# Performance work log

Measured on AMD Instinct MI355X. Metric: run time of the kernel, lower is better.

Reference implementation:

```python
import jax, jax.numpy as jnp
import numpy as np


def _conv(x, w, pad):
    return jax.lax.conv_general_dilated(x, w, (1, 1), [(pad, pad), (pad, pad)],
                                        dimension_numbers=('NCHW', 'OIHW', 'NCHW'))


def _cbs(x, w, s, b, pad):
    # Conv + (folded inference BatchNorm as per-channel affine) + SiLU
    y = _conv(x, w, pad) * s[None, :, None, None] + b[None, :, None, None]
    return y * jax.nn.sigmoid(y)


def _pixel_shuffle(x, r):
    N, C, H, W = x.shape
    c = C // (r * r)
    return x.reshape(N, c, r, r, H, W).transpose(0, 1, 4, 2, 5, 3).reshape(N, c, H * r, W * r)


def _pixel_unshuffle(x, r):
    N, C, H, W = x.shape
    h, w = H // r, W // r
    return x.reshape(N, C, h, r, w, r).transpose(0, 1, 3, 5, 2, 4).reshape(N, C * r * r, h, w)


def _carafe(x, dw, db, ew, eb, k, up):
    # Content-aware reassembly: predict per-pixel k*k kernels for up*up sub-positions,
    # softmax-normalize, then gather-multiply-accumulate over k*k neighborhoods.
    N, C, H, W = x.shape
    kt = _conv(x, dw, 0) + db[None, :, None, None]
    if k % 2 == 0:
        kt = jnp.pad(kt, ((0, 0), (0, 0), (k // 2, k // 2 - 1), (k // 2, k // 2 - 1)))
        kt = _conv(kt, ew, 0) + eb[None, :, None, None]
    else:
        kt = _conv(kt, ew, k // 2) + eb[None, :, None, None]
    kt = _pixel_shuffle(kt, up)                     # [N, k*k, H*up, W*up]
    kt = jax.nn.softmax(kt, axis=1)
    # non-overlapping unfold(step=up) -> [N, H, W, k*k, up*up]
    kt = kt.reshape(N, k * k, H, up, W, up).transpose(0, 2, 4, 1, 3, 5).reshape(N, H, W, k * k, up * up)
    if k % 2 == 0:
        xp = jnp.pad(x, ((0, 0), (0, 0), (k // 2, k // 2 - 1), (k // 2, k // 2 - 1)))
    else:
        xp = jnp.pad(x, ((0, 0), (0, 0), (k // 2, k // 2), (k // 2, k // 2)))
    # k*k sliding patches (k is a small static constant)
    patches = jnp.stack([xp[:, :, i:i + H, j:j + W] for i in range(k) for j in range(k)], axis=-1)
    patches = patches.transpose(0, 2, 3, 1, 4)      # [N, H, W, C, k*k]
    out = jnp.einsum('nhwck,nhwkr->nhwcr', patches, kt)  # [N, H, W, C, up*up]
    out = out.reshape(N, H, W, C * up * up).transpose(0, 3, 1, 2)
    return _pixel_shuffle(out, up)


def _forward(x, cv1_w, cv1_s, cv1_b, m1a_w, m1a_s, m1a_b, m1b_w, m1b_s, m1b_b,
             cvm2_w, cvm2_s, cvm2_b, u2_down_w, u2_down_b, u2_enc_w, u2_enc_b,
             m2a_w, m2a_s, m2a_b, m2b_w, m2b_s, m2b_b,
             cvm3_w, cvm3_s, cvm3_b, u3_down_w, u3_down_b, u3_enc_w, u3_enc_b,
             m3a_w, m3a_s, m3a_b, m3b_w, m3b_s, m3b_b, cv2_w, cv2_s, cv2_b):
    C = cv1_w.shape[0] // 2
    t = _cbs(x, cv1_w, cv1_s, cv1_b, 0)
    y, y0 = t[:, :C], t[:, C:]

    def bneck(z, wa, sa, ba, wb, sb, bb):  # shortcut=False, e=1.0
        return _cbs(_cbs(z, wa, sa, ba, 1), wb, sb, bb, 1)

    y1 = bneck(y0, m1a_w, m1a_s, m1a_b, m1b_w, m1b_s, m1b_b)
    y2 = _cbs(_pixel_unshuffle(y1, 2), cvm2_w, cvm2_s, cvm2_b, 0)
    y2 = _carafe(y2, u2_down_w, u2_down_b, u2_enc_w, u2_enc_b, 1, 2) + y1
    y2 = bneck(y2, m2a_w, m2a_s, m2a_b, m2b_w, m2b_s, m2b_b)
    y3 = _cbs(_pixel_unshuffle(y2, 4), cvm3_w, cvm3_s, cvm3_b, 0)
    y3 = _carafe(y3, u3_down_w, u3_down_b, u3_enc_w, u3_enc_b, 2, 4) + y2
    y3 = bneck(y3, m3a_w, m3a_s, m3a_b, m3b_w, m3b_s, m3b_b)
    return _cbs(jnp.concatenate([y, y0, y1, y2, y3], axis=1), cv2_w, cv2_s, cv2_b, 0)


def setup_inputs() -> dict:
    key = jax.random.key(0)
    ks = jax.random.split(key, 16)
    C = 128

    def cbs_p(k, co, ci, ksz):
        k1, k2, k3 = jax.random.split(k, 3)
        w = jax.random.normal(k1, (co, ci, ksz, ksz), jnp.float32) / np.sqrt(ci * ksz * ksz).astype(np.float32)
        s = 1.0 + 0.1 * jax.random.normal(k2, (co,), jnp.float32)
        b = 0.1 * jax.random.normal(k3, (co,), jnp.float32)
        return w, s, b

    d = {}
    d['x'] = jax.random.normal(ks[0], (8, 256, 128, 128), jnp.float32)
    d['cv1_w'], d['cv1_s'], d['cv1_b'] = cbs_p(ks[1], 2 * C, 256, 1)
    for name, kk in (('m1', ks[2]), ('m2', ks[3]), ('m3', ks[4])):
        ka, kb = jax.random.split(kk)
        d[name + 'a_w'], d[name + 'a_s'], d[name + 'a_b'] = cbs_p(ka, C, C, 3)
        d[name + 'b_w'], d[name + 'b_s'], d[name + 'b_b'] = cbs_p(kb, C, C, 3)
    d['cvm2_w'], d['cvm2_s'], d['cvm2_b'] = cbs_p(ks[5], C, 4 * C, 1)
    d['cvm3_w'], d['cvm3_s'], d['cvm3_b'] = cbs_p(ks[6], C, 16 * C, 1)
    d['u2_down_w'] = jax.random.normal(ks[7], (C // 4, C, 1, 1), jnp.float32) / np.sqrt(C).astype(np.float32)
    d['u2_down_b'] = 0.1 * jax.random.normal(ks[8], (C // 4,), jnp.float32)
    d['u2_enc_w'] = jax.random.normal(ks[9], (4, C // 4, 1, 1), jnp.float32) / np.sqrt(C // 4).astype(np.float32)
    d['u2_enc_b'] = 0.1 * jax.random.normal(ks[10], (4,), jnp.float32)
    d['u3_down_w'] = jax.random.normal(ks[11], (C // 4, C, 1, 1), jnp.float32) / np.sqrt(C).astype(np.float32)
    d['u3_down_b'] = 0.1 * jax.random.normal(ks[12], (C // 4,), jnp.float32)
    d['u3_enc_w'] = jax.random.normal(ks[13], (64, C // 4, 2, 2), jnp.float32) / np.sqrt((C // 4) * 4).astype(np.float32)
    d['u3_enc_b'] = 0.1 * jax.random.normal(ks[14], (64,), jnp.float32)
    d['cv2_w'], d['cv2_s'], d['cv2_b'] = cbs_p(ks[15], 256, 5 * C, 1)
    return d


def reference(x, cv1_w, cv1_s, cv1_b, m1a_w, m1a_s, m1a_b, m1b_w, m1b_s, m1b_b,
              cvm2_w, cvm2_s, cvm2_b, u2_down_w, u2_down_b, u2_enc_w, u2_enc_b,
              m2a_w, m2a_s, m2a_b, m2b_w, m2b_s, m2b_b,
              cvm3_w, cvm3_s, cvm3_b, u3_down_w, u3_down_b, u3_enc_w, u3_enc_b,
              m3a_w, m3a_s, m3a_b, m3b_w, m3b_s, m3b_b, cv2_w, cv2_s, cv2_b):
    return _forward(x, cv1_w, cv1_s, cv1_b, m1a_w, m1a_s, m1a_b, m1b_w, m1b_s, m1b_b,
                    cvm2_w, cvm2_s, cvm2_b, u2_down_w, u2_down_b, u2_enc_w, u2_enc_b,
                    m2a_w, m2a_s, m2a_b, m2b_w, m2b_s, m2b_b,
                    cvm3_w, cvm3_s, cvm3_b, u3_down_w, u3_down_b, u3_enc_w, u3_enc_b,
                    m3a_w, m3a_s, m3a_b, m3b_w, m3b_s, m3b_b, cv2_w, cv2_s, cv2_b)
```

## Files before the change

### kernel.cpp

```cpp
#include <hip/hip_runtime.h>

typedef unsigned short u16;
typedef short v8s __attribute__((ext_vector_type(8)));
typedef u16 v8u __attribute__((ext_vector_type(8)));
typedef float v4f __attribute__((ext_vector_type(4)));
typedef __bf16 v8bf __attribute__((ext_vector_type(8)));

__device__ __forceinline__ float bf2f(u16 u) {
    unsigned x = ((unsigned)u) << 16; float f; __builtin_memcpy(&f, &x, 4); return f;
}
__device__ __forceinline__ u16 f2bf(float f) {
    unsigned x; __builtin_memcpy(&x, &f, 4);
    x = x + 0x7FFFu + ((x >> 16) & 1u);
    return (u16)(x >> 16);
}
__device__ __forceinline__ float silu(float v) { return v / (1.f + __expf(-v)); }

__global__ void cvtw(const float* __restrict__ in, u16* __restrict__ out, int n) {
    int i = blockIdx.x * 256 + threadIdx.x;
    if (i < n) out[i] = f2bf(in[i]);
}
__global__ void wtrans3(const float* __restrict__ in, u16* __restrict__ out) {
    int i = blockIdx.x * 256 + threadIdx.x;
    if (i >= 147456) return;
    int tap = i % 9; int rem = i / 9; int ci = rem & 127; int co = rem >> 7;
    out[((tap * 128 + co) << 7) + ci] = f2bf(in[i]);
}
__global__ void wtrans_ps(const float* __restrict__ in, u16* __restrict__ out, int R2) {
    int i = blockIdx.x * 256 + threadIdx.x;
    int tap = i % R2; int rem = i / R2; int c = rem & 127; int co = rem >> 7;
    out[((tap * 128 + co) << 7) + c] = f2bf(in[i]);
}

__global__ __launch_bounds__(256) void nchw2nhwc(const float* __restrict__ in, u16* __restrict__ out) {
    __shared__ u16 tile[64][72];
    const int n = blockIdx.z, c0 = blockIdx.y * 64, p0 = blockIdx.x * 64;
#pragma unroll
    for (int rep = 0; rep < 16; ++rep) {
        int idx = rep * 256 + threadIdx.x;
        int c = idx >> 6, p = idx & 63;
        tile[c][p] = f2bf(in[((size_t)(n * 256 + c0 + c)) * 16384 + p0 + p]);
    }
    __syncthreads();
#pragma unroll
    for (int rep = 0; rep < 16; ++rep) {
        int idx = rep * 256 + threadIdx.x;
        int p = idx >> 6, c = idx & 63;
        out[((size_t)n * 16384 + p0 + p) * 256 + c0 + c] = tile[c][p];
    }
}

__global__ __launch_bounds__(256) void conv3_mfma(
    const u16* __restrict__ src, int c0, int srcC,
    const u16* __restrict__ wt,
    const float* __restrict__ scale, const float* __restrict__ bias,
    u16* __restrict__ out) {
    __shared__ u16 lds[3][128][40];
    const int n = blockIdx.y, h = blockIdx.x;
    const int tid = threadIdx.x;
    const int lane = tid & 63;
    const int wv = tid >> 6;
    const int r = lane & 15, q = lane >> 4;
    const int wr = wv >> 1, wc = wv & 1;

    v4f acc[4][4];
#pragma unroll
    for (int a = 0; a < 4; ++a)
#pragma unroll
        for (int b = 0; b < 4; ++b) acc[a][b] = (v4f){0.f, 0.f, 0.f, 0.f};

    const size_t rowstride = (size_t)128 * srcC;
    const u16* nbase = src + (size_t)n * 128 * rowstride + c0;

    for (int k0 = 0; k0 < 128; k0 += 32) {
        __syncthreads();
#pragma unroll
        for (int kh = 0; kh < 3; ++kh) {
            int hh = h + kh - 1;
            if ((unsigned)hh < 128u) {
                const u16* g = nbase + (size_t)hh * rowstride + k0;
#pragma unroll
                for (int it = 0; it < 2; ++it) {
                    int t = it * 256 + tid;
                    v8s val = *(const v8s*)(g + (size_t)(t >> 2) * srcC + (t & 3) * 8);
                    *(v8s*)&lds[kh][t >> 2][(t & 3) * 8] = val;
                }
            }
        }
        __syncthreads();
#pragma unroll
        for (int kh = 0; kh < 3; ++kh) {
            int hh = h + kh - 1;
            if ((unsigned)hh >= 128u) continue;
#pragma unroll
            for (int kw = 0; kw < 3; ++kw) {
                int tap = kh * 3 + kw;
                const u16* bb = wt + ((size_t)tap * 128 + wc * 64 + r) * 128 + k0 + q * 8;
                v8bf bfr[4];
#pragma unroll
                for (int nt = 0; nt < 4; ++nt)
                    bfr[nt] = __builtin_bit_cast(v8bf, *(const v8s*)(bb + nt * 16 * 128));
                v8bf afr[4];
#pragma unroll
                for (int mt = 0; mt < 4; ++mt) {
                    int p = wr * 64 + mt * 16 + r + kw - 1;
                    bool vp = (unsigned)p < 128u;
                    int pc = vp ? p : 0;
                    v8s av = *(const v8s*)&lds[kh][pc][q * 8];
                    if (!vp) av = (v8s){0, 0, 0, 0, 0, 0, 0, 0};
                    afr[mt] = __builtin_bit_cast(v8bf, av);
                }
#pragma unroll
                for (int mt = 0; mt < 4; ++mt)
#pragma unroll
                    for (int nt = 0; nt < 4; ++nt)
                        acc[mt][nt] = __builtin_amdgcn_mfma_f32_16x16x32_bf16(
                            afr[mt], bfr[nt], acc[mt][nt], 0, 0, 0);
            }
        }
    }

    const size_t obase = ((size_t)n * 128 + h) * 128;
#pragma unroll
    for (int nt = 0; nt < 4; ++nt) {
        int co = wc * 64 + nt * 16 + r;
        float s = scale[co], bi = bias[co];
#pragma unroll
        for (int mt = 0; mt < 4; ++mt) {
            int p = wr * 64 + mt * 16 + q * 4;
#pragma unroll
            for (int i = 0; i < 4; ++i) {
                float v = acc[mt][nt][i] * s + bi;
                out[(obase + p + i) * 128 + co] = f2bf(silu(v));
            }
        }
    }
}

__global__ __launch_bounds__(256) void conv1_mfma(
    const u16* __restrict__ src, int srcC,
    const u16* __restrict__ wt,
    const float* __restrict__ scale, const float* __restrict__ bias,
    u16* __restrict__ out, int Cout) {
    __shared__ u16 lds[128][40];
    const int n = blockIdx.z, co0 = blockIdx.y * 128, px0 = blockIdx.x * 128;
    const int tid = threadIdx.x;
    const int lane = tid & 63, wv = tid >> 6;
    const int r = lane & 15, q = lane >> 4;
    const int wr = wv >> 1, wc = wv & 1;

    v4f acc[4][4];
#pragma unroll
    for (int a = 0; a < 4; ++a)
#pragma unroll
        for (int b = 0; b < 4; ++b) acc[a][b] = (v4f){0.f, 0.f, 0.f, 0.f};

    const u16* abase = src + ((size_t)n * 16384 + px0) * srcC;

    for (int k0 = 0; k0 < srcC; k0 += 32) {
        __syncthreads();
#pragma unroll
        for (int it = 0; it < 2; ++it) {
            int t = it * 256 + tid;
            v8s val = *(const v8s*)(abase + (size_t)(t >> 2) * srcC + (t & 3) * 8 + k0);
            *(v8s*)&lds[t >> 2][(t & 3) * 8] = val;
        }
        __syncthreads();
        const u16* bb = wt + (size_t)(co0 + wc * 64 + r) * srcC + k0 + q * 8;
        v8bf bfr[4];
#pragma unroll
        for (int nt = 0; nt < 4; ++nt)
            bfr[nt] = __builtin_bit_cast(v8bf, *(const v8s*)(bb + (size_t)nt * 16 * srcC));
        v8bf afr[4];
#pragma unroll
        for (int mt = 0; mt < 4; ++mt)
            afr[mt] = __builtin_bit_cast(v8bf, *(const v8s*)&lds[wr * 64 + mt * 16 + r][q * 8]);
#pragma unroll
        for (int mt = 0; mt < 4; ++mt)
#pragma unroll
            for (int nt = 0; nt < 4; ++nt)
                acc[mt][nt] = __builtin_amdgcn_mfma_f32_16x16x32_bf16(
                    afr[mt], bfr[nt], acc[mt][nt], 0, 0, 0);
    }

#pragma unroll
    for (int nt = 0; nt < 4; ++nt) {
        int co = co0 + wc * 64 + nt * 16 + r;
        float s = scale[co], bi = bias[co];
#pragma unroll
        for (int mt = 0; mt < 4; ++mt) {
            int p = px0 + wr * 64 + mt * 16 + q * 4;
#pragma unroll
            for (int i = 0; i < 4; ++i) {
                float v = acc[mt][nt][i] * s + bi;
                out[((size_t)n * 16384 + p + i) * Cout + co] = f2bf(silu(v));
            }
        }
    }
}

__global__ __launch_bounds__(256) void cat_mfma(
    const u16* __restrict__ s0, const u16* __restrict__ s1,
    const u16* __restrict__ s2, const u16* __restrict__ s3,
    const u16* __restrict__ wt,
    const float* __restrict__ scale, const float* __restrict__ bias,
    float* __restrict__ out) {
    __shared__ u16 lds[128][40];
    const int n = blockIdx.z, co0 = blockIdx.y * 128, px0 = blockIdx.x * 128;
    const int tid = threadIdx.x;
    const int lane = tid & 63, wv = tid >> 6;
    const int r = lane & 15, q = lane >> 4;
    const int wr = wv >> 1, wc = wv & 1;

    v4f acc[4][4];
#pragma unroll
    for (int a = 0; a < 4; ++a)
#pragma unroll
        for (int b = 0; b < 4; ++b) acc[a][b] = (v4f){0.f, 0.f, 0.f, 0.f};

    const u16* srcs[4] = {s0, s1, s2, s3};
    const int sCq[4] = {256, 128, 128, 128};
    const int kbq[4] = {0, 256, 384, 512};

#pragma unroll
    for (int seg = 0; seg < 4; ++seg) {
        const int sc = sCq[seg];
        const u16* ab = srcs[seg] + ((size_t)n * 16384 + px0) * sc;
        for (int k0 = 0; k0 < sc; k0 += 32) {
            __syncthreads();
#pragma unroll
            for (int it = 0; it < 2; ++it) {
                int t = it * 256 + tid;
                v8s val = *(const v8s*)(ab + (size_t)(t >> 2) * sc + (t & 3) * 8 + k0);
                *(v8s*)&lds[t >> 2][(t & 3) * 8] = val;
            }
            __syncthreads();
            const u16* bb = wt + (size_t)(co0 + wc * 64 + r) * 640 + kbq[seg] + k0 + q * 8;
            v8bf bfr[4];
#pragma unroll
            for (int nt = 0; nt < 4; ++nt)
                bfr[nt] = __builtin_bit_cast(v8bf, *(const v8s*)(bb + nt * 16 * 640));
            v8bf afr[4];
#pragma unroll
            for (int mt = 0; mt < 4; ++mt)
                afr[mt] = __builtin_bit_cast(v8bf, *(const v8s*)&lds[wr * 64 + mt * 16 + r][q * 8]);
#pragma unroll
            for (int mt = 0; mt < 4; ++mt)
#pragma unroll
                for (int nt = 0; nt < 4; ++nt)
                    acc[mt][nt] = __builtin_amdgcn_mfma_f32_16x16x32_bf16(
                        afr[mt], bfr[nt], acc[mt][nt], 0, 0, 0);
        }
    }

#pragma unroll
    for (int nt = 0; nt < 4; ++nt) {
        int co = co0 + wc * 64 + nt * 16 + r;
        float s = scale[co], bi = bias[co];
#pragma unroll
        for (int mt = 0; mt < 4; ++mt) {
            int p = px0 + wr * 64 + mt * 16 + q * 4;
            v4f o;
#pragma unroll
            for (int i = 0; i < 4; ++i) o[i] = silu(acc[mt][nt][i] * s + bi);
            *(v4f*)(out + (size_t)(n * 256 + co) * 16384 + p) = o;
        }
    }
}

template <int KH, int KW, int S, int PAD, int CIN>
__global__ __launch_bounds__(256) void conv_mfma(
    const u16* __restrict__ src, int c0, int srcC,
    const u16* __restrict__ wt,
    const float* __restrict__ scale, const float* __restrict__ bias,
    u16* __restrict__ out, int Hin, int Win, int Wout, int Cout) {
    const int n = blockIdx.z;
    const int co0 = blockIdx.y * 64;
    const int hw0 = blockIdx.x * 64;
    const int tid = threadIdx.x;
    const int lane = tid & 63, wv = tid >> 6;
    const int r = lane & 15, q = lane >> 4;
    const int wr = wv >> 1, wc = wv & 1;

    const int m0 = hw0 + wr * 32 + r;
    const int m1 = m0 + 16;
    const int h0 = m0 / Wout, w0 = m0 - h0 * Wout;
    const int h1 = m1 / Wout, w1 = m1 - h1 * Wout;

    v4f acc00 = {0.f, 0.f, 0.f, 0.f}, acc01 = {0.f, 0.f, 0.f, 0.f};
    v4f acc10 = {0.f, 0.f, 0.f, 0.f}, acc11 = {0.f, 0.f, 0.f, 0.f};

    const u16* b0base = wt + (size_t)(co0 + wc * 32 + r) * CIN + q * 8;
    const size_t wtap = (size_t)Cout * CIN;

    int tap = 0;
#pragma unroll
    for (int kh = 0; kh < KH; ++kh)
#pragma unroll
        for (int kw = 0; kw < KW; ++kw, ++tap) {
            int ih0 = h0 * S + kh - PAD, iw0 = w0 * S + kw - PAD;
            int ih1 = h1 * S + kh - PAD, iw1 = w1 * S + kw - PAD;
            bool v0 = ((unsigned)ih0 < (unsigned)Hin) & ((unsigned)iw0 < (unsigned)Win);
            bool v1 = ((unsigned)ih1 < (unsigned)Hin) & ((unsigned)iw1 < (unsigned)Win);
            int p0i = v0 ? (n * Hin + ih0) * Win + iw0 : 0;
            int p1i = v1 ? (n * Hin + ih1) * Win + iw1 : 0;
            const u16* a0 = src + (size_t)p0i * srcC + c0 + q * 8;
            const u16* a1 = src + (size_t)p1i * srcC + c0 + q * 8;
            const u16* b0 = b0base + (size_t)tap * wtap;
            const u16* b1 = b0 + (size_t)16 * CIN;
#pragma unroll
            for (int k = 0; k < CIN; k += 32) {
                v8s za = {0, 0, 0, 0, 0, 0, 0, 0};
                v8s a0s = za, a1s = za;
                if (v0) a0s = *(const v8s*)(a0 + k);
                if (v1) a1s = *(const v8s*)(a1 + k);
                v8s b0s = *(const v8s*)(b0 + k);
                v8s b1s = *(const v8s*)(b1 + k);
                v8bf af0 = __builtin_bit_cast(v8bf, a0s);
                v8bf af1 = __builtin_bit_cast(v8bf, a1s);
                v8bf bw0 = __builtin_bit_cast(v8bf, b0s);
                v8bf bw1 = __builtin_bit_cast(v8bf, b1s);
                acc00 = __builtin_amdgcn_mfma_f32_16x16x32_bf16(af0, bw0, acc00, 0, 0, 0);
                acc01 = __builtin_amdgcn_mfma_f32_16x16x32_bf16(af0, bw1, acc01, 0, 0, 0);
                acc10 = __builtin_amdgcn_mfma_f32_16x16x32_bf16(af1, bw0, acc10, 0, 0, 0);
                acc11 = __builtin_amdgcn_mfma_f32_16x16x32_bf16(af1, bw1, acc11, 0, 0, 0);
            }
        }

    const int HWo = gridDim.x * 64;
#pragma unroll
    for (int ct = 0; ct < 2; ++ct) {
        v4f av0 = ct ? acc01 : acc00;
        v4f av1 = ct ? acc11 : acc10;
        int co = co0 + wc * 32 + ct * 16 + r;
        float s = scale[co], bb = bias[co];
        int mb = hw0 + wr * 32 + q * 4;
#pragma unroll
        for (int i = 0; i < 4; ++i) {
            float x0 = av0[i] * s + bb;
            float x1 = av1[i] * s + bb;
            out[((size_t)n * HWo + mb + i) * Cout + co] = f2bf(silu(x0));
            out[((size_t)n * HWo + mb + 16 + i) * Cout + co] = f2bf(silu(x1));
        }
    }
}

__global__ __launch_bounds__(256) void k_upadd(const u16* __restrict__ y2a,
                                               const u16* __restrict__ y1,
                                               u16* __restrict__ out) {
    int t = blockIdx.x * 256 + threadIdx.x;
    int cg = t & 15; int pix = t >> 4;
    int n = pix >> 14; int p = pix & 16383; int ho = p >> 7; int wo = p & 127;
    const u16* a = y2a + ((size_t)((n * 64 + (ho >> 1)) * 64 + (wo >> 1))) * 128 + cg * 8;
    const u16* b = y1 + (size_t)pix * 128 + cg * 8;
    v8s av = *(const v8s*)a;
    v8s bv = *(const v8s*)b;
    v8u o;
#pragma unroll
    for (int e = 0; e < 8; ++e) o[e] = f2bf(bf2f((u16)av[e]) + bf2f((u16)bv[e]));
    *(v8u*)(out + (size_t)pix * 128 + cg * 8) = o;
}

__global__ __launch_bounds__(256) void k_u3down(const u16* __restrict__ y3a,
                                                const float* __restrict__ w,
                                                const float* __restrict__ b,
                                                float* __restrict__ ktA) {
    int t = blockIdx.x * 256 + threadIdx.x;
    int co = t & 31; int pix = t >> 5;
    const u16* xr = y3a + (size_t)pix * 128;
    const float* wr = w + (size_t)co * 128;
    float acc = b[co];
#pragma unroll 16
    for (int k = 0; k < 128; ++k) acc += bf2f(xr[k]) * wr[k];
    ktA[t] = acc;
}

__global__ __launch_bounds__(256) void k_u3enc(const float* __restrict__ ktA,
                                               const float* __restrict__ ew,
                                               const float* __restrict__ eb,
                                               float* __restrict__ wtsm) {
    int t = blockIdx.x * 256 + threadIdx.x;
    int r = t & 15; int pix = t >> 4;
    int n = pix >> 10; int hw = pix & 1023; int h = hw >> 5; int w = hw & 31;
    float v[4];
#pragma unroll
    for (int kk = 0; kk < 4; ++kk) {
        int co = kk * 16 + r;
        float acc = eb[co];
#pragma unroll
        for (int dh = 0; dh < 2; ++dh)
#pragma unroll
            for (int dw = 0; dw < 2; ++dw) {
                int hh = h - 1 + dh, ww = w - 1 + dw;
                if (hh < 0 || ww < 0) continue;
                const float* kp = ktA + ((size_t)((n * 32 + hh) * 32 + ww)) * 32;
                const float* wp = ew + (size_t)co * 128 + dh * 2 + dw;
                for (int ci = 0; ci < 32; ++ci) acc += kp[ci] * wp[ci * 4];
            }
        v[kk] = acc;
    }
    float mx = fmaxf(fmaxf(v[0], v[1]), fmaxf(v[2], v[3]));
    float e0 = __expf(v[0] - mx), e1 = __expf(v[1] - mx), e2 = __expf(v[2] - mx), e3 = __expf(v[3] - mx);
    float inv = 1.f / (e0 + e1 + e2 + e3);
    float* o = wtsm + (size_t)t * 4;
    o[0] = e0 * inv; o[1] = e1 * inv; o[2] = e2 * inv; o[3] = e3 * inv;
}

__global__ __launch_bounds__(256) void k_carafe(const u16* __restrict__ y3a,
                                                const float* __restrict__ wtsm,
                                                const u16* __restrict__ y2,
                                                u16* __restrict__ out) {
    int t = blockIdx.x * 256 + threadIdx.x;
    int cg = t & 15; int pix = t >> 4;
    int n = pix >> 14; int p = pix & 16383; int ho = p >> 7; int wo = p & 127;
    int h = ho >> 2, i = ho & 3, w = wo >> 2, j = wo & 3, r = i * 4 + j;
    const float* wv = wtsm + ((size_t)((n * 1024 + h * 32 + w) * 16 + r)) * 4;
    v8s yv = *(const v8s*)(y2 + (size_t)pix * 128 + cg * 8);
    float acc[8];
#pragma unroll
    for (int e = 0; e < 8; ++e) acc[e] = bf2f((u16)yv[e]);
#pragma unroll
    for (int kk = 0; kk < 4; ++kk) {
        int ki = kk >> 1, kj = kk & 1;
        int hh = h + ki - 1, ww = w + kj - 1;
        if (hh < 0 || ww < 0) continue;
        float wk = wv[kk];
        v8s sv = *(const v8s*)(y3a + ((size_t)((n * 32 + hh) * 32 + ww)) * 128 + cg * 8);
#pragma unroll
        for (int e = 0; e < 8; ++e) acc[e] += wk * bf2f((u16)sv[e]);
    }
    v8u o;
#pragma unroll
    for (int e = 0; e < 8; ++e) o[e] = f2bf(acc[e]);
    *(v8u*)(out + (size_t)pix * 128 + cg * 8) = o;
}

extern "C" void kernel_launch(void* const* d_in, const int* in_sizes, int n_in,
                              void* d_out, int out_size, void* d_ws, size_t ws_size,
                              hipStream_t stream) {
    const float* x     = (const float*)d_in[0];
    const float* cv1_w = (const float*)d_in[1];
    const float* cv1_s = (const float*)d_in[2];
    const float* cv1_b = (const float*)d_in[3];
    const float* m1a_w = (const float*)d_in[4];
    const float* m1a_s = (const float*)d_in[5];
    const float* m1a_b = (const float*)d_in[6];
    const float* m1b_w = (const float*)d_in[7];
    const float* m1b_s = (const float*)d_in[8];
    const float* m1b_b = (const float*)d_in[9];
    const float* m2a_w = (const float*)d_in[10];
    const float* m2a_s = (const float*)d_in[11];
    const float* m2a_b = (const float*)d_in[12];
    const float* m2b_w = (const float*)d_in[13];
    const float* m2b_s = (const float*)d_in[14];
    const float* m2b_b = (const float*)d_in[15];
    const float* m3a_w = (const float*)d_in[16];
    const float* m3a_s = (const float*)d_in[17];
    const float* m3a_b = (const float*)d_in[18];
    const float* m3b_w = (const float*)d_in[19];
    const float* m3b_s = (const float*)d_in[20];
    const float* m3b_b = (const float*)d_in[21];
    const float* cvm2_w = (const float*)d_in[22];
    const float* cvm2_s = (const float*)d_in[23];
    const float* cvm2_b = (const float*)d_in[24];
    const float* cvm3_w = (const float*)d_in[25];
    const float* cvm3_s = (const float*)d_in[26];
    const float* cvm3_b = (const float*)d_in[27];
    const float* u3_down_w = (const float*)d_in[32];
    const float* u3_down_b = (const float*)d_in[33];
    const float* u3_enc_w  = (const float*)d_in[34];
    const float* u3_enc_b  = (const float*)d_in[35];
    const float* cv2_w = (const float*)d_in[36];
    const float* cv2_s = (const float*)d_in[37];
    const float* cv2_b = (const float*)d_in[38];

    char* ws = (char*)d_ws;
    u16* A    = (u16*)(ws + 0);
    u16* t    = (u16*)(ws + 67108864);
    u16* y1   = (u16*)(ws + 134217728);
    u16* bt   = (u16*)(ws + 167772160);
    u16* te   = (u16*)(ws + 201326592);
    u16* y2a  = (u16*)(ws + 234881024);
    u16* y3a  = (u16*)(ws + 243269632);
    float* ktA = (float*)(ws + 245366784);
    float* wts = (float*)(ws + 246415360);
    u16* w3t  = (u16*)(ws + 248512512);
    u16* wu2  = (u16*)(ws + 250281984);
    u16* wu4  = (u16*)(ws + 250413056);
    u16* wc1  = (u16*)(ws + 250937344);
    u16* wc2  = (u16*)(ws + 251068416);
    u16* y2 = A;
    u16* y3 = A + 16777216;

    dim3 B(256);
    wtrans3<<<576, B, 0, stream>>>(m1a_w, w3t + 0 * 147456);
    wtrans3<<<576, B, 0, stream>>>(m1b_w, w3t + 1 * 147456);
    wtrans3<<<576, B, 0, stream>>>(m2a_w, w3t + 2 * 147456);
    wtrans3<<<576, B, 0, stream>>>(m2b_w, w3t + 3 * 147456);
    wtrans3<<<576, B, 0, stream>>>(m3a_w, w3t + 4 * 147456);
    wtrans3<<<576, B, 0, stream>>>(m3b_w, w3t + 5 * 147456);
    wtrans_ps<<<256, B, 0, stream>>>(cvm2_w, wu2, 4);
    wtrans_ps<<<1024, B, 0, stream>>>(cvm3_w, wu4, 16);
    cvtw<<<256, B, 0, stream>>>(cv1_w, wc1, 65536);
    cvtw<<<640, B, 0, stream>>>(cv2_w, wc2, 163840);

    nchw2nhwc<<<dim3(256, 4, 8), B, 0, stream>>>(x, A);

    conv1_mfma<<<dim3(128, 2, 8), B, 0, stream>>>(A, 256, wc1, cv1_s, cv1_b, t, 256);

    conv3_mfma<<<dim3(128, 8), B, 0, stream>>>(t, 128, 256, w3t + 0 * 147456, m1a_s, m1a_b, bt);
    conv3_mfma<<<dim3(128, 8), B, 0, stream>>>(bt, 0, 128, w3t + 1 * 147456, m1b_s, m1b_b, y1);

    conv_mfma<2, 2, 2, 0, 128><<<dim3(64, 2, 8), B, 0, stream>>>(
        y1, 0, 128, wu2, cvm2_s, cvm2_b, y2a, 128, 128, 64, 128);

    k_upadd<<<8192, B, 0, stream>>>(y2a, y1, te);

    conv3_mfma<<<dim3(128, 8), B, 0, stream>>>(te, 0, 128, w3t + 2 * 147456, m2a_s, m2a_b, bt);
    conv3_mfma<<<dim3(128, 8), B, 0, stream>>>(bt, 0, 128, w3t + 3 * 147456, m2b_s, m2b_b, y2);

    conv_mfma<4, 4, 4, 0, 128><<<dim3(16, 2, 8), B, 0, stream>>>(
        y2, 0, 128, wu4, cvm3_s, cvm3_b, y3a, 128, 128, 32, 128);

    k_u3down<<<1024, B, 0, stream>>>(y3a, u3_down_w, u3_down_b, ktA);
    k_u3enc<<<512, B, 0, stream>>>(ktA, u3_enc_w, u3_enc_b, wts);
    k_carafe<<<8192, B, 0, stream>>>(y3a, wts, y2, te);

    conv3_mfma<<<dim3(128, 8), B, 0, stream>>>(te, 0, 128, w3t + 4 * 147456, m3a_s, m3a_b, bt);
    conv3_mfma<<<dim3(128, 8), B, 0, stream>>>(bt, 0, 128, w3t + 5 * 147456, m3b_s, m3b_b, y3);

    cat_mfma<<<dim3(128, 2, 8), B, 0, stream>>>(t, y1, y2, y3, wc2, cv2_s, cv2_b, (float*)d_out);
}
```

Before: 1.400 ms.

## Use direct global-to-LDS loads and widen K tile in conv GEMM kernels

Replaces the register-staged global-to-shared copies in the 3x3 conv, 1x1 conv and concat GEMM kernels with global_load_lds 16-byte direct transfers into unpadded LDS tiles. The 1x1 and concat kernels also move from a K step of 32 to 64, which halves the number of barrier pairs per reduction. Dropping the LDS row padding to fit the contiguous layout that direct loads need can bring back bank conflicts on the fragment reads.

```diff
diff --git a/kernel.cpp b/kernel.cpp
--- a/kernel.cpp
+++ b/kernel.cpp
@@ -16,6 +16,13 @@
 }
 __device__ __forceinline__ float silu(float v) { return v / (1.f + __expf(-v)); }
 
+__device__ __forceinline__ void gld16(const void* g, void* l) {
+    __builtin_amdgcn_global_load_lds(
+        (const __attribute__((address_space(1))) unsigned int*)(uintptr_t)g,
+        (__attribute__((address_space(3))) unsigned int*)(unsigned int)(uintptr_t)l,
+        16, 0, 0);
+}
+
 __global__ void cvtw(const float* __restrict__ in, u16* __restrict__ out, int n) {
     int i = blockIdx.x * 256 + threadIdx.x;
     if (i < n) out[i] = f2bf(in[i]);
@@ -55,7 +62,7 @@
     const u16* __restrict__ wt,
     const float* __restrict__ scale, const float* __restrict__ bias,
     u16* __restrict__ out) {
-    __shared__ u16 lds[3][128][40];
+    __shared__ u16 lds[3][128][32];
     const int n = blockIdx.y, h = blockIdx.x;
     const int tid = threadIdx.x;
     const int lane = tid & 63;
@@ -80,10 +87,11 @@
             if ((unsigned)hh < 128u) {
                 const u16* g = nbase + (size_t)hh * rowstride + k0;
 #pragma unroll
-                for (int it = 0; it < 2; ++it) {
-                    int t = it * 256 + tid;
-                    v8s val = *(const v8s*)(g + (size_t)(t >> 2) * srcC + (t & 3) * 8);
-                    *(v8s*)&lds[kh][t >> 2][(t & 3) * 8] = val;
+                for (int j = 0; j < 2; ++j) {
+                    int o = j * 4096 + tid * 16;
+                    int px = o >> 6, cb = o & 63;
+                    gld16((const char*)(g + (size_t)px * srcC) + cb,
+                          (char*)&lds[kh][0][0] + j * 4096 + wv * 1024);
                 }
             }
         }
@@ -142,7 +150,7 @@
     const u16* __restrict__ wt,
     const float* __restrict__ scale, const float* __restrict__ bias,
     u16* __restrict__ out, int Cout) {
-    __shared__ u16 lds[128][40];
+    __shared__ u16 lds[128][64];
     const int n = blockIdx.z, co0 = blockIdx.y * 128, px0 = blockIdx.x * 128;
     const int tid = threadIdx.x;
     const int lane = tid & 63, wv = tid >> 6;
@@ -157,30 +165,34 @@
 
     const u16* abase = src + ((size_t)n * 16384 + px0) * srcC;
 
-    for (int k0 = 0; k0 < srcC; k0 += 32) {
+    for (int k0 = 0; k0 < srcC; k0 += 64) {
         __syncthreads();
 #pragma unroll
-        for (int it = 0; it < 2; ++it) {
-            int t = it * 256 + tid;
-            v8s val = *(const v8s*)(abase + (size_t)(t >> 2) * srcC + (t & 3) * 8 + k0);
-            *(v8s*)&lds[t >> 2][(t & 3) * 8] = val;
+        for (int j = 0; j < 4; ++j) {
+            int o = j * 4096 + tid * 16;
+            int px = o >> 7, cb = o & 127;
+            gld16((const char*)(abase + (size_t)px * srcC + k0) + cb,
+                  (char*)&lds[0][0] + j * 4096 + wv * 1024);
         }
         __syncthreads();
-        const u16* bb = wt + (size_t)(co0 + wc * 64 + r) * srcC + k0 + q * 8;
-        v8bf bfr[4];
-#pragma unroll
-        for (int nt = 0; nt < 4; ++nt)
-            bfr[nt] = __builtin_bit_cast(v8bf, *(const v8s*)(bb + (size_t)nt * 16 * srcC));
-        v8bf afr[4];
-#pragma unroll
-        for (int mt = 0; mt < 4; ++mt)
-            afr[mt] = __builtin_bit_cast(v8bf, *(const v8s*)&lds[wr * 64 + mt * 16 + r][q * 8]);
-#pragma unroll
-        for (int mt = 0; mt < 4; ++mt)
+#pragma unroll
+        for (int s = 0; s < 2; ++s) {
+            const u16* bb = wt + (size_t)(co0 + wc * 64 + r) * srcC + k0 + s * 32 + q * 8;
+            v8bf bfr[4];
 #pragma unroll
             for (int nt = 0; nt < 4; ++nt)
-                acc[mt][nt] = __builtin_amdgcn_mfma_f32_16x16x32_bf16(
-                    afr[mt], bfr[nt], acc[mt][nt], 0, 0, 0);
+                bfr[nt] = __builtin_bit_cast(v8bf, *(const v8s*)(bb + (size_t)nt * 16 * srcC));
+            v8bf afr[4];
+#pragma unroll
+            for (int mt = 0; mt < 4; ++mt)
+                afr[mt] = __builtin_bit_cast(v8bf, *(const v8s*)&lds[wr * 64 + mt * 16 + r][s * 32 + q * 8]);
+#pragma unroll
+            for (int mt = 0; mt < 4; ++mt)
+#pragma unroll
+                for (int nt = 0; nt < 4; ++nt)
+                    acc[mt][nt] = __builtin_amdgcn_mfma_f32_16x16x32_bf16(
+                        afr[mt], bfr[nt], acc[mt][nt], 0, 0, 0);
+        }
     }
 
 #pragma unroll
@@ -205,7 +217,7 @@
     const u16* __restrict__ wt,
     const float* __restrict__ scale, const float* __restrict__ bias,
     float* __restrict__ out) {
-    __shared__ u16 lds[128][40];
+    __shared__ u16 lds[128][64];
     const int n = blockIdx.z, co0 = blockIdx.y * 128, px0 = blockIdx.x * 128;
     const int tid = threadIdx.x;
     const int lane = tid & 63, wv = tid >> 6;
@@ -226,30 +238,34 @@
     for (int seg = 0; seg < 4; ++seg) {
         const int sc = sCq[seg];
         const u16* ab = srcs[seg] + ((size_t)n * 16384 + px0) * sc;
-        for (int k0 = 0; k0 < sc; k0 += 32) {
+        for (int k0 = 0; k0 < sc; k0 += 64) {
             __syncthreads();
 #pragma unroll
-            for (int it = 0; it < 2; ++it) {
-                int t = it * 256 + tid;
-                v8s val = *(const v8s*)(ab + (size_t)(t >> 2) * sc + (t & 3) * 8 + k0);
-                *(v8s*)&lds[t >> 2][(t & 3) * 8] = val;
+            for (int j = 0; j < 4; ++j) {
+                int o = j * 4096 + tid * 16;
+                int px = o >> 7, cb = o & 127;
+                gld16((const char*)(ab + (size_t)px * sc + k0) + cb,
+                      (char*)&lds[0][0] + j * 4096 + wv * 1024);
             }
             __syncthreads();
-            const u16* bb = wt + (size_t)(co0 + wc * 64 + r) * 640 + kbq[seg] + k0 + q * 8;
-            v8bf bfr[4];
-#pragma unroll
-            for (int nt = 0; nt < 4; ++nt)
-                bfr[nt] = __builtin_bit_cast(v8bf, *(const v8s*)(bb + nt * 16 * 640));
-            v8bf afr[4];
-#pragma unroll
-            for (int mt = 0; mt < 4; ++mt)
-                afr[mt] = __builtin_bit_cast(v8bf, *(const v8s*)&lds[wr * 64 + mt * 16 + r][q * 8]);
-#pragma unroll
-            for (int mt = 0; mt < 4; ++mt)
+#pragma unroll
+            for (int s = 0; s < 2; ++s) {
+                const u16* bb = wt + (size_t)(co0 + wc * 64 + r) * 640 + kbq[seg] + k0 + s * 32 + q * 8;
+                v8bf bfr[4];
 #pragma unroll
                 for (int nt = 0; nt < 4; ++nt)
-                    acc[mt][nt] = __builtin_amdgcn_mfma_f32_16x16x32_bf16(
-                        afr[mt], bfr[nt], acc[mt][nt], 0, 0, 0);
+                    bfr[nt] = __builtin_bit_cast(v8bf, *(const v8s*)(bb + nt * 16 * 640));
+                v8bf afr[4];
+#pragma unroll
+                for (int mt = 0; mt < 4; ++mt)
+                    afr[mt] = __builtin_bit_cast(v8bf, *(const v8s*)&lds[wr * 64 + mt * 16 + r][s * 32 + q * 8]);
+#pragma unroll
+                for (int mt = 0; mt < 4; ++mt)
+#pragma unroll
+                    for (int nt = 0; nt < 4; ++nt)
+                        acc[mt][nt] = __builtin_amdgcn_mfma_f32_16x16x32_bf16(
+                            afr[mt], bfr[nt], acc[mt][nt], 0, 0, 0);
+            }
         }
     }
 
```

Result: faster. 1.354 ms (-3.3%).

## Drop LDS staging in conv kernels and load MFMA operands directly from global

Applied to the files above, without the earlier changes.

Removes shared-memory staging and the __syncthreads barriers from the 3x3 conv, 1x1 conv and concat GEMM kernels, so each lane reads its A-fragments straight from global memory (relying on L1/L2 for reuse across waves). The 1x1 kernel also processes two 32-wide K slices per loop iteration. This removes barrier stalls and LDS traffic, but increases global/cache load traffic: each A row is read by both column-waves, and the 3x3 kernel re-reads rows per kw shift.

```diff
diff --git a/kernel.cpp b/kernel.cpp
--- a/kernel.cpp
+++ b/kernel.cpp
@@ -55,11 +55,9 @@
     const u16* __restrict__ wt,
     const float* __restrict__ scale, const float* __restrict__ bias,
     u16* __restrict__ out) {
-    __shared__ u16 lds[3][128][40];
     const int n = blockIdx.y, h = blockIdx.x;
     const int tid = threadIdx.x;
-    const int lane = tid & 63;
-    const int wv = tid >> 6;
+    const int lane = tid & 63, wv = tid >> 6;
     const int r = lane & 15, q = lane >> 4;
     const int wr = wv >> 1, wc = wv & 1;
 
@@ -72,30 +70,23 @@
     const size_t rowstride = (size_t)128 * srcC;
     const u16* nbase = src + (size_t)n * 128 * rowstride + c0;
 
+    bool rv[3];
+    const u16* row[3];
+#pragma unroll
+    for (int kh = 0; kh < 3; ++kh) {
+        int hh = h + kh - 1;
+        rv[kh] = (unsigned)hh < 128u;
+        row[kh] = nbase + (size_t)(rv[kh] ? hh : 0) * rowstride;
+    }
+
     for (int k0 = 0; k0 < 128; k0 += 32) {
-        __syncthreads();
 #pragma unroll
         for (int kh = 0; kh < 3; ++kh) {
-            int hh = h + kh - 1;
-            if ((unsigned)hh < 128u) {
-                const u16* g = nbase + (size_t)hh * rowstride + k0;
-#pragma unroll
-                for (int it = 0; it < 2; ++it) {
-                    int t = it * 256 + tid;
-                    v8s val = *(const v8s*)(g + (size_t)(t >> 2) * srcC + (t & 3) * 8);
-                    *(v8s*)&lds[kh][t >> 2][(t & 3) * 8] = val;
-                }
-            }
-        }
-        __syncthreads();
-#pragma unroll
-        for (int kh = 0; kh < 3; ++kh) {
-            int hh = h + kh - 1;
-            if ((unsigned)hh >= 128u) continue;
+            if (!rv[kh]) continue;
+            const u16* rbase = row[kh] + k0 + q * 8;
 #pragma unroll
             for (int kw = 0; kw < 3; ++kw) {
-                int tap = kh * 3 + kw;
-                const u16* bb = wt + ((size_t)tap * 128 + wc * 64 + r) * 128 + k0 + q * 8;
+                const u16* bb = wt + ((size_t)(kh * 3 + kw) * 128 + wc * 64 + r) * 128 + k0 + q * 8;
                 v8bf bfr[4];
 #pragma unroll
                 for (int nt = 0; nt < 4; ++nt)
@@ -104,10 +95,9 @@
 #pragma unroll
                 for (int mt = 0; mt < 4; ++mt) {
                     int p = wr * 64 + mt * 16 + r + kw - 1;
-                    bool vp = (unsigned)p < 128u;
-                    int pc = vp ? p : 0;
-                    v8s av = *(const v8s*)&lds[kh][pc][q * 8];
-                    if (!vp) av = (v8s){0, 0, 0, 0, 0, 0, 0, 0};
+                    int pc = p < 0 ? 0 : (p > 127 ? 127 : p);
+                    v8s av = *(const v8s*)(rbase + (size_t)pc * srcC);
+                    if (p != pc) av = (v8s){0, 0, 0, 0, 0, 0, 0, 0};
                     afr[mt] = __builtin_bit_cast(v8bf, av);
                 }
 #pragma unroll
@@ -142,7 +132,6 @@
     const u16* __restrict__ wt,
     const float* __restrict__ scale, const float* __restrict__ bias,
     u16* __restrict__ out, int Cout) {
-    __shared__ u16 lds[128][40];
     const int n = blockIdx.z, co0 = blockIdx.y * 128, px0 = blockIdx.x * 128;
     const int tid = threadIdx.x;
     const int lane = tid & 63, wv = tid >> 6;
@@ -155,32 +144,28 @@
 #pragma unroll
         for (int b = 0; b < 4; ++b) acc[a][b] = (v4f){0.f, 0.f, 0.f, 0.f};
 
-    const u16* abase = src + ((size_t)n * 16384 + px0) * srcC;
-
-    for (int k0 = 0; k0 < srcC; k0 += 32) {
-        __syncthreads();
-#pragma unroll
-        for (int it = 0; it < 2; ++it) {
-            int t = it * 256 + tid;
-            v8s val = *(const v8s*)(abase + (size_t)(t >> 2) * srcC + (t & 3) * 8 + k0);
-            *(v8s*)&lds[t >> 2][(t & 3) * 8] = val;
-        }
-        __syncthreads();
-        const u16* bb = wt + (size_t)(co0 + wc * 64 + r) * srcC + k0 + q * 8;
-        v8bf bfr[4];
-#pragma unroll
-        for (int nt = 0; nt < 4; ++nt)
-            bfr[nt] = __builtin_bit_cast(v8bf, *(const v8s*)(bb + (size_t)nt * 16 * srcC));
-        v8bf afr[4];
-#pragma unroll
-        for (int mt = 0; mt < 4; ++mt)
-            afr[mt] = __builtin_bit_cast(v8bf, *(const v8s*)&lds[wr * 64 + mt * 16 + r][q * 8]);
-#pragma unroll
-        for (int mt = 0; mt < 4; ++mt)
+    const u16* abase = src + ((size_t)n * 16384 + px0 + wr * 64) * srcC + q * 8;
+    const u16* bbase = wt + (size_t)(co0 + wc * 64 + r) * srcC + q * 8;
+
+    for (int k0 = 0; k0 < srcC; k0 += 64) {
+#pragma unroll
+        for (int s = 0; s < 2; ++s) {
+            int k = k0 + s * 32;
+            v8bf bfr[4];
 #pragma unroll
             for (int nt = 0; nt < 4; ++nt)
-                acc[mt][nt] = __builtin_amdgcn_mfma_f32_16x16x32_bf16(
-                    afr[mt], bfr[nt], acc[mt][nt], 0, 0, 0);
+                bfr[nt] = __builtin_bit_cast(v8bf, *(const v8s*)(bbase + k + (size_t)nt * 16 * srcC));
+            v8bf afr[4];
+#pragma unroll
+            for (int mt = 0; mt < 4; ++mt)
+                afr[mt] = __builtin_bit_cast(v8bf, *(const v8s*)(abase + k + (size_t)(mt * 16 + r) * srcC));
+#pragma unroll
+            for (int mt = 0; mt < 4; ++mt)
+#pragma unroll
+                for (int nt = 0; nt < 4; ++nt)
+                    acc[mt][nt] = __builtin_amdgcn_mfma_f32_16x16x32_bf16(
+                        afr[mt], bfr[nt], acc[mt][nt], 0, 0, 0);
+        }
     }
 
 #pragma unroll
@@ -205,7 +190,6 @@
     const u16* __restrict__ wt,
     const float* __restrict__ scale, const float* __restrict__ bias,
     float* __restrict__ out) {
-    __shared__ u16 lds[128][40];
     const int n = blockIdx.z, co0 = blockIdx.y * 128, px0 = blockIdx.x * 128;
     const int tid = threadIdx.x;
     const int lane = tid & 63, wv = tid >> 6;
@@ -221,21 +205,14 @@
     const u16* srcs[4] = {s0, s1, s2, s3};
     const int sCq[4] = {256, 128, 128, 128};
     const int kbq[4] = {0, 256, 384, 512};
+    const u16* brow = wt + (size_t)(co0 + wc * 64 + r) * 640 + q * 8;
 
 #pragma unroll
     for (int seg = 0; seg < 4; ++seg) {
         const int sc = sCq[seg];
-        const u16* ab = srcs[seg] + ((size_t)n * 16384 + px0) * sc;
+        const u16* ab = srcs[seg] + ((size_t)n * 16384 + px0 + wr * 64) * sc + q * 8;
         for (int k0 = 0; k0 < sc; k0 += 32) {
-            __syncthreads();
-#pragma unroll
-            for (int it = 0; it < 2; ++it) {
-                int t = it * 256 + tid;
-                v8s val = *(const v8s*)(ab + (size_t)(t >> 2) * sc + (t & 3) * 8 + k0);
-                *(v8s*)&lds[t >> 2][(t & 3) * 8] = val;
-            }
-            __syncthreads();
-            const u16* bb = wt + (size_t)(co0 + wc * 64 + r) * 640 + kbq[seg] + k0 + q * 8;
+            const u16* bb = brow + kbq[seg] + k0;
             v8bf bfr[4];
 #pragma unroll
             for (int nt = 0; nt < 4; ++nt)
@@ -243,7 +220,7 @@
             v8bf afr[4];
 #pragma unroll
             for (int mt = 0; mt < 4; ++mt)
-                afr[mt] = __builtin_bit_cast(v8bf, *(const v8s*)&lds[wr * 64 + mt * 16 + r][q * 8]);
+                afr[mt] = __builtin_bit_cast(v8bf, *(const v8s*)(ab + k0 + (size_t)(mt * 16 + r) * sc));
 #pragma unroll
             for (int mt = 0; mt < 4; ++mt)
 #pragma unroll
```

Measured after the change: 1.666 ms. +19.0%, slower.
